# Performance work log

Measured on AMD Instinct MI355X. Metric: run time of the kernel, lower is better.

## Reference

```python
import jax, jax.numpy as jnp
import numpy as np

FACTOR = 3
N_HEADS = 8


def prob_attention(q, k, v, key):
    # q,k,v: [B, L, H, D]  (Informer ProbAttention, mask_flag falsy, scale=None)
    B, L_Q, H, D = q.shape
    L_K = k.shape[1]
    Q = jnp.swapaxes(q, 1, 2)  # [B,H,L_Q,D]
    K = jnp.swapaxes(k, 1, 2)
    V = jnp.swapaxes(v, 1, 2)
    U_part = min(FACTOR * int(np.ceil(np.log(L_K))), L_K)  # sampled keys per query
    u = min(FACTOR * int(np.ceil(np.log(L_Q))), L_Q)       # active (top) queries
    idx = jax.random.randint(key, (L_Q, U_part), 0, L_K)   # shared across B,H like torch.randint
    K_sample = K[:, :, idx, :]                              # [B,H,L_Q,U_part,D] gather
    QK_sample = jnp.einsum('bhld,bhlsd->bhls', Q, K_sample)
    M = QK_sample.max(axis=-1) - QK_sample.sum(axis=-1) / L_K  # sparsity measure
    _, top_idx = jax.lax.top_k(M, u)                        # [B,H,u]
    Q_reduce = jnp.take_along_axis(Q, top_idx[..., None], axis=2)  # [B,H,u,D]
    scale = 1.0 / np.sqrt(D)
    scores = jnp.einsum('bhud,bhkd->bhuk', Q_reduce, K) * scale     # [B,H,u,L_K]
    attn = jax.nn.softmax(scores, axis=-1)
    out_top = jnp.einsum('bhuk,bhkd->bhud', attn, V)
    # initial context: mean of V over keys, broadcast to every query position
    context = jnp.broadcast_to(V.mean(axis=2, keepdims=True), (B, H, L_Q, D))
    bi = jnp.arange(B)[:, None, None]
    hi = jnp.arange(H)[None, :, None]
    context = context.at[bi, hi, top_idx].set(out_top)
    return jnp.swapaxes(context, 1, 2)  # [B,L_Q,H,D]


def attention_layer(xq, xk, xv, wq, bq, wk, bk, wv, bv, wo, bo, key):
    B, Lq, dm = xq.shape
    Lk = xk.shape[1]
    dk = dm // N_HEADS
    q = (xq @ wq + bq).reshape(B, Lq, N_HEADS, dk)
    k = (xk @ wk + bk).reshape(B, Lk, N_HEADS, dk)
    v = (xv @ wv + bv).reshape(B, Lk, N_HEADS, dk)
    out = prob_attention(q, k, v, key).reshape(B, Lq, dm)
    return out @ wo + bo


def setup_inputs() -> dict:
    key = jax.random.key(0)
    ks = jax.random.split(key, 20)
    B, Ld, Lp, dm = 4, 4096, 4096, 512
    inp = {
        'xs': jax.random.normal(ks[0], (B, Ld + Lp, dm), jnp.float32),
        'xd': jax.random.normal(ks[1], (B, Ld, dm), jnp.float32),
        'xp': jax.random.normal(ks[2], (B, Lp, dm), jnp.float32),
    }
    names = ['w0q', 'w0k', 'w0v', 'w0o', 'b0q', 'b0k', 'b0v', 'b0o',
             'w1q', 'w1k', 'w1v', 'w1o', 'b1q', 'b1k', 'b1v', 'b1o']
    for i, n in enumerate(names):
        if n.startswith('w'):
            inp[n] = jax.random.normal(ks[3 + i], (dm, dm), jnp.float32) * 0.02
        else:
            inp[n] = jnp.zeros((dm,), jnp.float32)
    return inp


def reference(xs, xd, xp,
              w0q, w0k, w0v, w0o, b0q, b0k, b0v, b0o,
              w1q, w1k, w1v, w1o, b1q, b1k, b1v, b1o):
    # dropout layers are identity in eval mode
    xp2 = attention_layer(xp, xd, xd, w0q, b0q, w0k, b0k, w0v, b0v, w0o, b0o,
                          jax.random.key(42))
    xd2 = attention_layer(xd, xp2, xp2, w1q, b1q, w1k, b1k, w1v, b1v, w1o, b1o,
                          jax.random.key(43))
    return xs + jnp.concatenate([xd2, xp2], axis=1)
```

## Files before the change

### kernel.cpp

```cpp
#include <hip/hip_runtime.h>
#include <math.h>

#define NB 4
#define SEQ 4096
#define DM 512
#define NH 8
#define HD 64
#define UU 27
#define NIDX (SEQ*UU)
#define NC 32
#define CS 128
#define PSTRIDE 66

typedef unsigned int u32;
typedef unsigned short u16;
typedef __attribute__((ext_vector_type(8))) short short8;
typedef __attribute__((ext_vector_type(4))) short short4v;
typedef __attribute__((ext_vector_type(4))) float f32x4;

__host__ __device__ inline u32 rotl32(u32 x, u32 r){ return (x<<r)|(x>>(32u-r)); }

__host__ __device__ inline void threefry2x32(u32 k0, u32 k1, u32 x0, u32 x1, u32* o0, u32* o1)
{
  u32 ks[3] = { k0, k1, k0 ^ k1 ^ 0x1BD11BDAu };
  x0 += ks[0]; x1 += ks[1];
  const u32 rotA[4] = {13u,15u,26u,6u};
  const u32 rotB[4] = {17u,29u,16u,24u};
  for (int i = 0; i < 5; i++) {
    const u32* rot = (i & 1) ? rotB : rotA;
    for (int j = 0; j < 4; j++) { x0 += x1; x1 = rotl32(x1, rot[j]); x1 ^= x0; }
    x0 += ks[(i+1)%3];
    x1 += ks[(i+2)%3] + (u32)(i+1);
  }
  *o0 = x0; *o1 = x1;
}

__global__ __launch_bounds__(256) void gen_idx_kernel(u32 k2a, u32 k2b, int* __restrict__ idx)
{
  int i = blockIdx.x * 256 + threadIdx.x;
  if (i >= NIDX) return;
  u32 o0, o1;
  threefry2x32(k2a, k2b, 0u, (u32)i, &o0, &o1);
  idx[i] = (int)((o0 ^ o1) & (SEQ - 1));
}

__device__ inline u16 f2bf_rne(float f) {
  u32 u = __float_as_uint(f);
  return (u16)((u + 0x7fffu + ((u >> 16) & 1u)) >> 16);
}
__device__ inline void f2bf_split(float f, u16& hi, u16& lo) {
  u32 u = __float_as_uint(f);
  u16 h = (u16)(u >> 16);
  float hf = __uint_as_float(((u32)h) << 16);
  hi = h;
  lo = f2bf_rne(f - hf);
}

__global__ __launch_bounds__(256) void conv_split(const float* __restrict__ X,
                                                  u16* __restrict__ hi, u16* __restrict__ lo)
{
  long g = (long)blockIdx.x * 256 + threadIdx.x;
  float4 x0 = ((const float4*)X)[g * 2];
  float4 x1 = ((const float4*)X)[g * 2 + 1];
  union { short8 v; u16 s[8]; } h, l;
  float xv[8] = { x0.x, x0.y, x0.z, x0.w, x1.x, x1.y, x1.z, x1.w };
  #pragma unroll
  for (int e = 0; e < 8; e++) f2bf_split(xv[e], h.s[e], l.s[e]);
  ((short8*)hi)[g] = h.v;
  ((short8*)lo)[g]  = l.v;
}

struct WPtrs { const float* w[8]; };
__global__ __launch_bounds__(256) void convw_kernel(WPtrs wp, u16* __restrict__ outp)
{
  const int n  = blockIdx.x;
  const int wi = blockIdx.y;
  const float* W = wp.w[wi];
  u16* hi = outp + (long)wi * 262144 + n * DM;
  u16* lo = hi + 8L * 262144;
  for (int k = threadIdx.x; k < DM; k += 256) {
    u16 h, l;
    f2bf_split(W[(long)k * DM + n], h, l);
    hi[k] = h; lo[k] = l;
  }
}

__device__ inline void gld16(const u16* g, short* l) {
  __builtin_amdgcn_global_load_lds((const u32*)g, (u32*)l, 16, 0, 0);
}

__global__ __launch_bounds__(256) void gemm_bf(
    const u16* __restrict__ Ah, const u16* __restrict__ Al,
    const u16* __restrict__ Wh, const u16* __restrict__ Wl,
    const float* __restrict__ bias0, const float* __restrict__ bias1,
    float* __restrict__ C0, float* __restrict__ C1,
    const float* __restrict__ resid, int rowJump)
{
  __shared__ short LB[2][4][4096];

  const int t  = threadIdx.x;
  const int rb = blockIdx.x * 128;
  const int cb = blockIdx.y * 128;

  const int slot = (t & 7) ^ ((t >> 3) & 7);
  const int c8   = slot & 3;
  const int rloc = ((t >> 3) << 1) + (slot >> 2);
  const u16* sAh = Ah + (long)(rb + rloc) * DM + c8 * 8;
  const u16* sWh = Wh + (long)(cb + rloc) * DM + c8 * 8;
  const u16* sAl = Al + (long)(rb + rloc) * DM + c8 * 8;
  const u16* sWl = Wl + (long)(cb + rloc) * DM + c8 * 8;
  const int w512 = (t >> 6) * 512;

  const int lane = t & 63, wv = t >> 6;
  const int wm = (wv & 1) * 64, wn = (wv >> 1) * 64;
  const int fr = lane & 15, fq = lane >> 4;
  const int fsw = (fr >> 1) * 64 + ((((fr & 1) * 4 + fq) ^ (fr >> 1)) * 8);
  const int a_off = wm * 32 + fsw;
  const int b_off = wn * 32 + fsw;

  f32x4 acc[4][4];
  #pragma unroll
  for (int i = 0; i < 4; i++)
    #pragma unroll
    for (int j = 0; j < 4; j++) acc[i][j] = (f32x4)(0.f);

#define STAGE(buf, k0s) do { \
    gld16(sAh + (k0s),               &LB[buf][0][w512]); \
    gld16(sAh + (k0s) + 64 * DM,     &LB[buf][0][w512 + 2048]); \
    gld16(sWh + (k0s),               &LB[buf][1][w512]); \
    gld16(sWh + (k0s) + 64 * DM,     &LB[buf][1][w512 + 2048]); \
    gld16(sAl + (k0s),               &LB[buf][2][w512]); \
    gld16(sAl + (k0s) + 64 * DM,     &LB[buf][2][w512 + 2048]); \
    gld16(sWl + (k0s),               &LB[buf][3][w512]); \
    gld16(sWl + (k0s) + 64 * DM,     &LB[buf][3][w512 + 2048]); \
  } while (0)

  STAGE(0, 0);
  #pragma unroll 2
  for (int ks = 0; ks < 16; ks++) {
    const int cur = ks & 1;
    asm volatile("s_waitcnt vmcnt(0)" ::: "memory");
    __syncthreads();
    if (ks < 15) STAGE(cur ^ 1, (ks + 1) * 32);

    short8 a_hi[4], b_hi[4], a_lo[4], b_lo[4];
    #pragma unroll
    for (int i = 0; i < 4; i++) a_hi[i] = *(const short8*)&LB[cur][0][a_off + i * 512];
    #pragma unroll
    for (int j = 0; j < 4; j++) b_hi[j] = *(const short8*)&LB[cur][1][b_off + j * 512];
    #pragma unroll
    for (int i = 0; i < 4; i++) a_lo[i] = *(const short8*)&LB[cur][2][a_off + i * 512];
    #pragma unroll
    for (int j = 0; j < 4; j++) b_lo[j] = *(const short8*)&LB[cur][3][b_off + j * 512];

    #pragma unroll
    for (int i = 0; i < 4; i++)
      #pragma unroll
      for (int j = 0; j < 4; j++)
        acc[i][j] = __builtin_amdgcn_mfma_f32_16x16x32_bf16(a_hi[i], b_hi[j], acc[i][j], 0, 0, 0);
    #pragma unroll
    for (int i = 0; i < 4; i++)
      #pragma unroll
      for (int j = 0; j < 4; j++) {
        acc[i][j] = __builtin_amdgcn_mfma_f32_16x16x32_bf16(a_hi[i], b_lo[j], acc[i][j], 0, 0, 0);
        acc[i][j] = __builtin_amdgcn_mfma_f32_16x16x32_bf16(a_lo[i], b_hi[j], acc[i][j], 0, 0, 0);
      }
  }
#undef STAGE

  #pragma unroll
  for (int j = 0; j < 4; j++) {
    int col = cb + wn + j * 16 + fr;
    const float* bp = (col < DM) ? bias0 : bias1;
    float* Cp = (col < DM) ? C0 : C1;
    int cc = col & (DM - 1);
    float bv = bp[cc];
    #pragma unroll
    for (int i = 0; i < 4; i++) {
      int row0 = rb + wm + i * 16 + fq * 4;
      #pragma unroll
      for (int r = 0; r < 4; r++) {
        int row = row0 + r;
        long off = (long)row * DM + (long)(row >> 12) * rowJump + cc;
        float v = acc[i][j][r] + bv;
        if (resid) v += resid[off];
        Cp[off] = v;
      }
    }
  }
}

__global__ __launch_bounds__(256) void mscore_kernel(const float* __restrict__ Q, const float* __restrict__ K,
                                                     const int* __restrict__ idx, float* __restrict__ M)
{
  const int wl = threadIdx.x >> 6, lane = threadIdx.x & 63;
  const int bl = blockIdx.x * 4 + wl;
  const int b = bl >> 12, l = bl & (SEQ - 1);

  const float4* qp = (const float4*)(Q + (long)bl * DM + lane * 8);
  float4 q0 = qp[0], q1 = qp[1];

  const int* ip = idx + l * UU;
  int idxv = ip[lane < UU ? lane : 0];
  int chv = idxv >> 9;

  const float* kb = K + ((long)b << 12) * DM + lane * 8;
  float mx = -INFINITY, sm = 0.f;
  #pragma unroll 1
  for (int c = 0; c < 8; c++) {
    unsigned long long msk = __ballot(chv == c) & ((1ull << UU) - 1ull);
    while (msk) {
      int s = __builtin_ctzll(msk);
      msk &= msk - 1;
      int kl = __shfl(idxv, s, 64);
      const float4* kp = (const float4*)(kb + (long)kl * DM);
      float4 k0 = kp[0], k1 = kp[1];
      float dot;
      dot = q0.x * k0.x;
      dot = fmaf(q0.y, k0.y, dot); dot = fmaf(q0.z, k0.z, dot); dot = fmaf(q0.w, k0.w, dot);
      dot = fmaf(q1.x, k1.x, dot); dot = fmaf(q1.y, k1.y, dot);
      dot = fmaf(q1.z, k1.z, dot); dot = fmaf(q1.w, k1.w, dot);
      dot += __shfl_xor(dot, 1, 64);
      dot += __shfl_xor(dot, 2, 64);
      dot += __shfl_xor(dot, 4, 64);
      mx = fmaxf(mx, dot);
      sm += dot;
    }
  }
  if ((lane & 7) == 0) {
    int h = lane >> 3;
    M[(((long)b * NH + h) << 12) + l] = mx - sm * (1.0f / (float)SEQ);
  }
}

__global__ __launch_bounds__(256) void topk_kernel(const float* __restrict__ M, int* __restrict__ topidx)
{
  __shared__ float vals[SEQ];
  __shared__ float rv[256];
  __shared__ int   ri[256];
  const float* m = M + (long)blockIdx.x * SEQ;
  for (int i = threadIdx.x; i < SEQ; i += 256) vals[i] = m[i];
  __syncthreads();
  for (int it = 0; it < UU; it++) {
    float bv = -INFINITY; int bi = 0x7fffffff;
    for (int i = threadIdx.x; i < SEQ; i += 256) {
      float v = vals[i];
      if (v > bv) { bv = v; bi = i; }
    }
    rv[threadIdx.x] = bv; ri[threadIdx.x] = bi;
    __syncthreads();
    for (int s = 128; s > 0; s >>= 1) {
      if (threadIdx.x < s) {
        float ov = rv[threadIdx.x + s]; int oi = ri[threadIdx.x + s];
        if (ov > rv[threadIdx.x] || (ov == rv[threadIdx.x] && oi < ri[threadIdx.x])) {
          rv[threadIdx.x] = ov; ri[threadIdx.x] = oi;
        }
      }
      __syncthreads();
    }
    if (threadIdx.x == 0) { topidx[blockIdx.x * UU + it] = ri[0]; vals[ri[0]] = -INFINITY; }
    __syncthreads();
  }
}

__global__ __launch_bounds__(512) void vmean_partial(const float* __restrict__ V, float* __restrict__ vsum)
{
  int b = blockIdx.x >> 5, chunk = blockIdx.x & 31;
  int c = threadIdx.x;
  const float* p = V + ((long)b * SEQ + chunk * 128) * DM + c;
  float s = 0.f;
  for (int l = 0; l < 128; l++) s += p[(long)l * DM];
  atomicAdd(&vsum[b * DM + c], s);
}

__global__ __launch_bounds__(256) void attn_part(const float* __restrict__ Q, const float* __restrict__ K,
                                                 const float* __restrict__ V, const int* __restrict__ topidx,
                                                 float* __restrict__ partial)
{
  __shared__ float Qs[UU][HD];
  __shared__ float S[UU][CS];
  __shared__ float Vt[CS][HD];
  __shared__ float m_s[UU], l_s[UU];

  const int t = threadIdx.x;
  const int bh = blockIdx.x;
  const int chunk = blockIdx.y;
  const int b = bh >> 3, h = bh & 7;
  const long kbase = ((long)(b << 12) + chunk * CS) * DM + h * HD;
  const int* tp = topidx + bh * UU;

  for (int i = t; i < UU * HD; i += 256) {
    int u = i >> 6, d = i & 63;
    Qs[u][d] = Q[((long)(b << 12) + tp[u]) * DM + h * HD + d];
  }
  for (int i = t; i < CS * (HD / 4); i += 256) {
    int row = i >> 4, c4 = (i & 15) << 2;
    *(float4*)&Vt[row][c4] = *(const float4*)(V + kbase + (long)row * DM + c4);
  }
  __syncthreads();

  {
    const int l = t >> 1, half = t & 1, d0 = half * 32;
    const float* kp = K + kbase + (long)l * DM + d0;
    float4 kr[8];
    #pragma unroll
    for (int j = 0; j < 8; j++) kr[j] = *(const float4*)(kp + j * 4);
    #pragma unroll 1
    for (int u = 0; u < UU; u++) {
      const float4* qf = (const float4*)&Qs[u][d0];
      float dot = 0.f;
      #pragma unroll
      for (int j = 0; j < 8; j++) {
        float4 q = qf[j];
        dot = fmaf(q.x, kr[j].x, dot); dot = fmaf(q.y, kr[j].y, dot);
        dot = fmaf(q.z, kr[j].z, dot); dot = fmaf(q.w, kr[j].w, dot);
      }
      float tot = dot + __shfl_xor(dot, 1, 64);
      if (half == 0) S[u][l] = tot * 0.125f;
    }
  }
  __syncthreads();

  {
    const int u = t >> 3, il = t & 7;
    if (u < UU) {
      float mx = -INFINITY;
      for (int l = il; l < CS; l += 8) mx = fmaxf(mx, S[u][l]);
      #pragma unroll
      for (int m = 1; m < 8; m <<= 1) mx = fmaxf(mx, __shfl_xor(mx, m, 64));
      float ps = 0.f;
      for (int l = il; l < CS; l += 8) {
        float e = expf(S[u][l] - mx);
        S[u][l] = e;
        ps += e;
      }
      #pragma unroll
      for (int m = 1; m < 8; m <<= 1) ps += __shfl_xor(ps, m, 64);
      if (il == 0) { m_s[u] = mx; l_s[u] = ps; }
    }
  }
  __syncthreads();

  {
    const int d = t & 63, g = t >> 6;
    for (int u = g; u < UU; u += 4) {
      float acc = 0.f;
      #pragma unroll 4
      for (int l = 0; l < CS; l += 4) {
        float4 p4 = *(const float4*)&S[u][l];
        acc = fmaf(p4.x, Vt[l][d],     acc);
        acc = fmaf(p4.y, Vt[l + 1][d], acc);
        acc = fmaf(p4.z, Vt[l + 2][d], acc);
        acc = fmaf(p4.w, Vt[l + 3][d], acc);
      }
      float* pp = partial + (((long)bh * NC + chunk) * UU + u) * PSTRIDE;
      pp[2 + d] = acc;
      if (d == 0) { pp[0] = m_s[u]; pp[1] = l_s[u]; }
    }
  }
}

__global__ __launch_bounds__(64) void attn_merge_bf(const float* __restrict__ partial, const int* __restrict__ topidx,
                                                    u16* __restrict__ hi, u16* __restrict__ lo)
{
  int g = blockIdx.x;
  int bh = g / UU, u = g % UU;
  int b = bh >> 3, h = bh & 7;
  int d = threadIdx.x;
  float M = -INFINITY, S = 0.f, acc = 0.f;
  for (int c = 0; c < NC; c++) {
    const float* pp = partial + (((long)bh * NC + c) * UU + u) * PSTRIDE;
    float mc = pp[0], sc = pp[1], a = pp[2 + d];
    if (mc > M) {
      float r = expf(M - mc);
      acc *= r; S *= r; M = mc;
    }
    float w = expf(mc - M);
    acc = fmaf(a, w, acc);
    S = fmaf(sc, w, S);
  }
  int ql = topidx[g];
  long o = ((long)(b << 12) + ql) * DM + h * HD + d;
  u16 hv, lv;
  f2bf_split(acc / S, hv, lv);
  hi[o] = hv; lo[o] = lv;
}

__global__ __launch_bounds__(256) void ctx_fill_bf(const float* __restrict__ vsum,
                                                   u16* __restrict__ hi, u16* __restrict__ lo)
{
  long g = (long)blockIdx.x * 256 + threadIdx.x;
  int b = (int)(g >> 19);
  int c4 = (int)(g & 127);
  float4 v = ((const float4*)vsum)[b * 128 + c4];
  const float s = 1.0f / (float)SEQ;
  float xv[4] = { v.x * s, v.y * s, v.z * s, v.w * s };
  union { short4v v; u16 s[4]; } h, l;
  #pragma unroll
  for (int e = 0; e < 4; e++) f2bf_split(xv[e], h.s[e], l.s[e]);
  ((short4v*)hi)[g] = h.v;
  ((short4v*)lo)[g]  = l.v;
}

__global__ __launch_bounds__(256) void add_upper(const float* __restrict__ xs, const float* __restrict__ xp2,
                                                 float* __restrict__ out)
{
  long g = (long)blockIdx.x * 256 + threadIdx.x;
  int b = (int)(g >> 19);
  long rem = g & 524287;
  float4 p = ((const float4*)xp2)[g];
  long o = ((long)b * 8192 + SEQ) * 128 + rem;
  float4 x = ((const float4*)xs)[o];
  x.x += p.x; x.y += p.y; x.z += p.z; x.w += p.w;
  ((float4*)out)[o] = x;
}

extern "C" void kernel_launch(void* const* d_in, const int* in_sizes, int n_in,
                              void* d_out, int out_size, void* d_ws, size_t ws_size,
                              hipStream_t stream)
{
  const float* xs  = (const float*)d_in[0];
  const float* xd  = (const float*)d_in[1];
  const float* xp  = (const float*)d_in[2];
  const float* w0q = (const float*)d_in[3];
  const float* w0k = (const float*)d_in[4];
  const float* w0v = (const float*)d_in[5];
  const float* w0o = (const float*)d_in[6];
  const float* b0q = (const float*)d_in[7];
  const float* b0k = (const float*)d_in[8];
  const float* b0v = (const float*)d_in[9];
  const float* b0o = (const float*)d_in[10];
  const float* w1q = (const float*)d_in[11];
  const float* w1k = (const float*)d_in[12];
  const float* w1v = (const float*)d_in[13];
  const float* w1o = (const float*)d_in[14];
  const float* b1q = (const float*)d_in[15];
  const float* b1k = (const float*)d_in[16];
  const float* b1v = (const float*)d_in[17];
  const float* b1o = (const float*)d_in[18];
  float* out = (float*)d_out;

  const long BIG = (long)NB * SEQ * DM;
  float* A  = (float*)d_ws;
  float* Bb = A  + BIG;
  float* Cc = Bb + BIG;
  float* Dd = Cc + BIG;
  float* ex = Dd + BIG;
  float* Pq  = ex + BIG;
  float* Pkv = Pq + BIG;

  int*   idxbuf = (int*)ex;
  float* Mbuf   = ex + NIDX;
  int*   topidx = (int*)(Mbuf + (long)NB * NH * SEQ);
  float* vsum   = (float*)(topidx + NB * NH * UU);
  u16*   wpl    = (u16*)(ex + (1 << 20));

  u16* Pq_hi  = (u16*)Pq;   u16* Pq_lo  = Pq_hi  + BIG;
  u16* Pkv_hi = (u16*)Pkv;  u16* Pkv_lo = Pkv_hi + BIG;
  auto whi = [&](int i){ return wpl + (long)i * 262144; };
  auto wlo = [&](int i){ return wpl + 8L * 262144 + (long)i * 262144; };

  dim3 gg(128, 4);
  dim3 gkv(128, 8);
  dim3 ag(NB * NH, NC);
  u32 k2a, k2b;

  WPtrs wp;
  wp.w[0] = w0q; wp.w[1] = w0k; wp.w[2] = w0v; wp.w[3] = w0o;
  wp.w[4] = w1q; wp.w[5] = w1k; wp.w[6] = w1v; wp.w[7] = w1o;
  convw_kernel<<<dim3(512, 8), 256, 0, stream>>>(wp, wpl);

  threefry2x32(0u, 42u, 0u, 1u, &k2a, &k2b);
  gen_idx_kernel<<<(NIDX + 255) / 256, 256, 0, stream>>>(k2a, k2b, idxbuf);
  conv_split<<<4096, 256, 0, stream>>>(xp, Pq_hi, Pq_lo);
  conv_split<<<4096, 256, 0, stream>>>(xd, Pkv_hi, Pkv_lo);
  gemm_bf<<<gg, 256, 0, stream>>>(Pq_hi,  Pq_lo,  whi(0), wlo(0), b0q, b0q, A,  A,  nullptr, 0);
  gemm_bf<<<gkv, 256, 0, stream>>>(Pkv_hi, Pkv_lo, whi(1), wlo(1), b0k, b0v, Bb, Cc, nullptr, 0);
  mscore_kernel<<<NB * SEQ / 4, 256, 0, stream>>>(A, Bb, idxbuf, Mbuf);
  topk_kernel<<<NB * NH, 256, 0, stream>>>(Mbuf, topidx);
  hipMemsetAsync(vsum, 0, NB * DM * sizeof(float), stream);
  vmean_partial<<<NB * 32, 512, 0, stream>>>(Cc, vsum);
  attn_part<<<ag, 256, 0, stream>>>(A, Bb, Cc, topidx, Dd);
  ctx_fill_bf<<<8192, 256, 0, stream>>>(vsum, Pq_hi, Pq_lo);
  attn_merge_bf<<<NB * NH * UU, 64, 0, stream>>>(Dd, topidx, Pq_hi, Pq_lo);
  gemm_bf<<<gg, 256, 0, stream>>>(Pq_hi, Pq_lo, whi(3), wlo(3), b0o, b0o, Bb, Bb, nullptr, 0);
  add_upper<<<8192, 256, 0, stream>>>(xs, Bb, out);

  threefry2x32(0u, 43u, 0u, 1u, &k2a, &k2b);
  gen_idx_kernel<<<(NIDX + 255) / 256, 256, 0, stream>>>(k2a, k2b, idxbuf);
  gemm_bf<<<gg, 256, 0, stream>>>(Pkv_hi, Pkv_lo, whi(4), wlo(4), b1q, b1q, A, A, nullptr, 0);
  conv_split<<<4096, 256, 0, stream>>>(Bb, Pq_hi, Pq_lo);
  gemm_bf<<<gkv, 256, 0, stream>>>(Pq_hi, Pq_lo, whi(5), wlo(5), b1k, b1v, Cc, Dd, nullptr, 0);
  mscore_kernel<<<NB * SEQ / 4, 256, 0, stream>>>(A, Cc, idxbuf, Mbuf);
  topk_kernel<<<NB * NH, 256, 0, stream>>>(Mbuf, topidx);
  hipMemsetAsync(vsum, 0, NB * DM * sizeof(float), stream);
  vmean_partial<<<NB * 32, 512, 0, stream>>>(Dd, vsum);
  attn_part<<<ag, 256, 0, stream>>>(A, Cc, Dd, topidx, Bb);
  ctx_fill_bf<<<8192, 256, 0, stream>>>(vsum, Pkv_hi, Pkv_lo);
  attn_merge_bf<<<NB * NH * UU, 64, 0, stream>>>(Bb, topidx, Pkv_hi, Pkv_lo);
  gemm_bf<<<gg, 256, 0, stream>>>(Pkv_hi, Pkv_lo, whi(7), wlo(7), b1o, b1o, out, out, xs, SEQ * DM);
}
```

Measured before the change: 833.4 us.

## Deepen GEMM LDS pipeline to four stages and drop split precision where tolerable

Rewrites the bf16 split GEMM to keep four LDS stages in flight, using partial vmcnt waits and raw barriers, and raises wave priority around MFMA blocks. Adds a template switch that skips the low-part loads and cross-term MFMAs. That cheaper path is used for the second layer's V projection and its output projection, which splits the fused K/V GEMM in two. The high part now uses round-to-nearest, so the one-term product is more accurate. The aim is to hide load latency and cut MFMA work, at the cost of more LDS per block and lower precision on those GEMMs.

```diff
diff --git a/kernel.cpp b/kernel.cpp
--- a/kernel.cpp
+++ b/kernel.cpp
@@ -49,8 +49,7 @@
   return (u16)((u + 0x7fffu + ((u >> 16) & 1u)) >> 16);
 }
 __device__ inline void f2bf_split(float f, u16& hi, u16& lo) {
-  u32 u = __float_as_uint(f);
-  u16 h = (u16)(u >> 16);
+  u16 h = f2bf_rne(f);
   float hf = __uint_as_float(((u32)h) << 16);
   hi = h;
   lo = f2bf_rne(f - hf);
@@ -89,6 +88,7 @@
   __builtin_amdgcn_global_load_lds((const u32*)g, (u32*)l, 16, 0, 0);
 }
 
+template<int SPLIT>
 __global__ __launch_bounds__(256) void gemm_bf(
     const u16* __restrict__ Ah, const u16* __restrict__ Al,
     const u16* __restrict__ Wh, const u16* __restrict__ Wl,
@@ -96,7 +96,8 @@
     float* __restrict__ C0, float* __restrict__ C1,
     const float* __restrict__ resid, int rowJump)
 {
-  __shared__ short LB[2][4][4096];
+  __shared__ short LBh[4 * 8192];
+  __shared__ short LBl[SPLIT ? 4 * 8192 : 8];
 
   const int t  = threadIdx.x;
   const int rb = blockIdx.x * 128;
@@ -107,8 +108,8 @@
   const int rloc = ((t >> 3) << 1) + (slot >> 2);
   const u16* sAh = Ah + (long)(rb + rloc) * DM + c8 * 8;
   const u16* sWh = Wh + (long)(cb + rloc) * DM + c8 * 8;
-  const u16* sAl = Al + (long)(rb + rloc) * DM + c8 * 8;
-  const u16* sWl = Wl + (long)(cb + rloc) * DM + c8 * 8;
+  const u16* sAl = SPLIT ? (Al + (long)(rb + rloc) * DM + c8 * 8) : sAh;
+  const u16* sWl = SPLIT ? (Wl + (long)(cb + rloc) * DM + c8 * 8) : sWh;
   const int w512 = (t >> 6) * 512;
 
   const int lane = t & 63, wv = t >> 6;
@@ -124,49 +125,73 @@
     #pragma unroll
     for (int j = 0; j < 4; j++) acc[i][j] = (f32x4)(0.f);
 
-#define STAGE(buf, k0s) do { \
-    gld16(sAh + (k0s),               &LB[buf][0][w512]); \
-    gld16(sAh + (k0s) + 64 * DM,     &LB[buf][0][w512 + 2048]); \
-    gld16(sWh + (k0s),               &LB[buf][1][w512]); \
-    gld16(sWh + (k0s) + 64 * DM,     &LB[buf][1][w512 + 2048]); \
-    gld16(sAl + (k0s),               &LB[buf][2][w512]); \
-    gld16(sAl + (k0s) + 64 * DM,     &LB[buf][2][w512 + 2048]); \
-    gld16(sWl + (k0s),               &LB[buf][3][w512]); \
-    gld16(sWl + (k0s) + 64 * DM,     &LB[buf][3][w512 + 2048]); \
-  } while (0)
-
-  STAGE(0, 0);
-  #pragma unroll 2
-  for (int ks = 0; ks < 16; ks++) {
-    const int cur = ks & 1;
-    asm volatile("s_waitcnt vmcnt(0)" ::: "memory");
-    __syncthreads();
-    if (ks < 15) STAGE(cur ^ 1, (ks + 1) * 32);
-
-    short8 a_hi[4], b_hi[4], a_lo[4], b_lo[4];
+  auto stage = [&](int s, int k0s) {
+    short* dh = &LBh[s * 8192 + w512];
+    gld16(sAh + k0s,           dh);
+    gld16(sAh + k0s + 64 * DM, dh + 2048);
+    gld16(sWh + k0s,           dh + 4096);
+    gld16(sWh + k0s + 64 * DM, dh + 4096 + 2048);
+    if (SPLIT) {
+      short* dl = &LBl[s * 8192 + w512];
+      gld16(sAl + k0s,           dl);
+      gld16(sAl + k0s + 64 * DM, dl + 2048);
+      gld16(sWl + k0s,           dl + 4096);
+      gld16(sWl + k0s + 64 * DM, dl + 4096 + 2048);
+    }
+  };
+
+  auto compute = [&](int s) {
+    const short* bh = &LBh[s * 8192];
+    short8 a_hi[4], b_hi[4];
     #pragma unroll
-    for (int i = 0; i < 4; i++) a_hi[i] = *(const short8*)&LB[cur][0][a_off + i * 512];
+    for (int i = 0; i < 4; i++) a_hi[i] = *(const short8*)&bh[a_off + i * 512];
     #pragma unroll
-    for (int j = 0; j < 4; j++) b_hi[j] = *(const short8*)&LB[cur][1][b_off + j * 512];
-    #pragma unroll
-    for (int i = 0; i < 4; i++) a_lo[i] = *(const short8*)&LB[cur][2][a_off + i * 512];
-    #pragma unroll
-    for (int j = 0; j < 4; j++) b_lo[j] = *(const short8*)&LB[cur][3][b_off + j * 512];
-
+    for (int j = 0; j < 4; j++) b_hi[j] = *(const short8*)&bh[4096 + b_off + j * 512];
+    __builtin_amdgcn_s_setprio(1);
     #pragma unroll
     for (int i = 0; i < 4; i++)
       #pragma unroll
       for (int j = 0; j < 4; j++)
         acc[i][j] = __builtin_amdgcn_mfma_f32_16x16x32_bf16(a_hi[i], b_hi[j], acc[i][j], 0, 0, 0);
-    #pragma unroll
-    for (int i = 0; i < 4; i++)
-      #pragma unroll
-      for (int j = 0; j < 4; j++) {
-        acc[i][j] = __builtin_amdgcn_mfma_f32_16x16x32_bf16(a_hi[i], b_lo[j], acc[i][j], 0, 0, 0);
-        acc[i][j] = __builtin_amdgcn_mfma_f32_16x16x32_bf16(a_lo[i], b_hi[j], acc[i][j], 0, 0, 0);
-      }
-  }
-#undef STAGE
+    __builtin_amdgcn_s_setprio(0);
+    if (SPLIT) {
+      const short* bl = &LBl[s * 8192];
+      short8 a_lo[4], b_lo[4];
+      #pragma unroll
+      for (int i = 0; i < 4; i++) a_lo[i] = *(const short8*)&bl[a_off + i * 512];
+      #pragma unroll
+      for (int j = 0; j < 4; j++) b_lo[j] = *(const short8*)&bl[4096 + b_off + j * 512];
+      __builtin_amdgcn_s_setprio(1);
+      #pragma unroll
+      for (int i = 0; i < 4; i++)
+        #pragma unroll
+        for (int j = 0; j < 4; j++) {
+          acc[i][j] = __builtin_amdgcn_mfma_f32_16x16x32_bf16(a_hi[i], b_lo[j], acc[i][j], 0, 0, 0);
+          acc[i][j] = __builtin_amdgcn_mfma_f32_16x16x32_bf16(a_lo[i], b_hi[j], acc[i][j], 0, 0, 0);
+        }
+      __builtin_amdgcn_s_setprio(0);
+    }
+  };
+
+  stage(0, 0); stage(1, 32); stage(2, 64);
+
+  #pragma unroll
+  for (int k = 0; k < 14; ++k) {
+    if (SPLIT) asm volatile("s_waitcnt vmcnt(16)" ::: "memory");
+    else       asm volatile("s_waitcnt vmcnt(8)"  ::: "memory");
+    __builtin_amdgcn_s_barrier();
+    if (k < 13) stage((k + 3) & 3, (k + 3) * 32);
+    compute(k & 3);
+    asm volatile("s_waitcnt lgkmcnt(0)" ::: "memory");
+  }
+  if (SPLIT) asm volatile("s_waitcnt vmcnt(8)" ::: "memory");
+  else       asm volatile("s_waitcnt vmcnt(4)" ::: "memory");
+  __builtin_amdgcn_s_barrier();
+  compute(2);
+  asm volatile("s_waitcnt lgkmcnt(0)" ::: "memory");
+  asm volatile("s_waitcnt vmcnt(0)" ::: "memory");
+  __builtin_amdgcn_s_barrier();
+  compute(3);
 
   #pragma unroll
   for (int j = 0; j < 4; j++) {
@@ -474,8 +499,8 @@
   gen_idx_kernel<<<(NIDX + 255) / 256, 256, 0, stream>>>(k2a, k2b, idxbuf);
   conv_split<<<4096, 256, 0, stream>>>(xp, Pq_hi, Pq_lo);
   conv_split<<<4096, 256, 0, stream>>>(xd, Pkv_hi, Pkv_lo);
-  gemm_bf<<<gg, 256, 0, stream>>>(Pq_hi,  Pq_lo,  whi(0), wlo(0), b0q, b0q, A,  A,  nullptr, 0);
-  gemm_bf<<<gkv, 256, 0, stream>>>(Pkv_hi, Pkv_lo, whi(1), wlo(1), b0k, b0v, Bb, Cc, nullptr, 0);
+  gemm_bf<1><<<gg, 256, 0, stream>>>(Pq_hi,  Pq_lo,  whi(0), wlo(0), b0q, b0q, A,  A,  nullptr, 0);
+  gemm_bf<1><<<gkv, 256, 0, stream>>>(Pkv_hi, Pkv_lo, whi(1), wlo(1), b0k, b0v, Bb, Cc, nullptr, 0);
   mscore_kernel<<<NB * SEQ / 4, 256, 0, stream>>>(A, Bb, idxbuf, Mbuf);
   topk_kernel<<<NB * NH, 256, 0, stream>>>(Mbuf, topidx);
   hipMemsetAsync(vsum, 0, NB * DM * sizeof(float), stream);
@@ -483,14 +508,15 @@
   attn_part<<<ag, 256, 0, stream>>>(A, Bb, Cc, topidx, Dd);
   ctx_fill_bf<<<8192, 256, 0, stream>>>(vsum, Pq_hi, Pq_lo);
   attn_merge_bf<<<NB * NH * UU, 64, 0, stream>>>(Dd, topidx, Pq_hi, Pq_lo);
-  gemm_bf<<<gg, 256, 0, stream>>>(Pq_hi, Pq_lo, whi(3), wlo(3), b0o, b0o, Bb, Bb, nullptr, 0);
+  gemm_bf<1><<<gg, 256, 0, stream>>>(Pq_hi, Pq_lo, whi(3), wlo(3), b0o, b0o, Bb, Bb, nullptr, 0);
   add_upper<<<8192, 256, 0, stream>>>(xs, Bb, out);
 
   threefry2x32(0u, 43u, 0u, 1u, &k2a, &k2b);
   gen_idx_kernel<<<(NIDX + 255) / 256, 256, 0, stream>>>(k2a, k2b, idxbuf);
-  gemm_bf<<<gg, 256, 0, stream>>>(Pkv_hi, Pkv_lo, whi(4), wlo(4), b1q, b1q, A, A, nullptr, 0);
+  gemm_bf<1><<<gg, 256, 0, stream>>>(Pkv_hi, Pkv_lo, whi(4), wlo(4), b1q, b1q, A, A, nullptr, 0);
   conv_split<<<4096, 256, 0, stream>>>(Bb, Pq_hi, Pq_lo);
-  gemm_bf<<<gkv, 256, 0, stream>>>(Pq_hi, Pq_lo, whi(5), wlo(5), b1k, b1v, Cc, Dd, nullptr, 0);
+  gemm_bf<1><<<gg, 256, 0, stream>>>(Pq_hi, Pq_lo, whi(5), wlo(5), b1k, b1k, Cc, Cc, nullptr, 0);
+  gemm_bf<0><<<gg, 256, 0, stream>>>(Pq_hi, Pq_lo, whi(6), wlo(6), b1v, b1v, Dd, Dd, nullptr, 0);
   mscore_kernel<<<NB * SEQ / 4, 256, 0, stream>>>(A, Cc, idxbuf, Mbuf);
   topk_kernel<<<NB * NH, 256, 0, stream>>>(Mbuf, topidx);
   hipMemsetAsync(vsum, 0, NB * DM * sizeof(float), stream);
@@ -498,5 +524,5 @@
   attn_part<<<ag, 256, 0, stream>>>(A, Cc, Dd, topidx, Bb);
   ctx_fill_bf<<<8192, 256, 0, stream>>>(vsum, Pkv_hi, Pkv_lo);
   attn_merge_bf<<<NB * NH * UU, 64, 0, stream>>>(Bb, topidx, Pkv_hi, Pkv_lo);
-  gemm_bf<<<gg, 256, 0, stream>>>(Pkv_hi, Pkv_lo, whi(7), wlo(7), b1o, b1o, out, out, xs, SEQ * DM);
-}
+  gemm_bf<0><<<gg, 256, 0, stream>>>(Pkv_hi, Pkv_lo, whi(7), wlo(7), b1o, b1o, out, out, xs, SEQ * DM);
+}
```

Measured after the change: 882.9 us. 5.9% more time.

## Exploit low-rank context structure to replace output and K/V projection GEMMs

Applied to the files above, without the earlier changes.

The ProbAttention context is a per-batch constant row (the mean of V) except at the 27 selected query rows per head. The output projection therefore becomes one row-vector matmul per batch, plus sparse per-row corrections computed by small projection kernels, broadcast fills and atomic scatter-adds. The second layer's K/V projections reuse the same structure, applied to the first layer's output, so three full 16k×512×512 GEMMs and a conversion pass are replaced by small matvecs and scatters. The changes are that f2bf_split now rounds the high half to nearest, fp32 scalar matvecs replace the split-bf16 MFMA path for those terms, and scatter_add relies on float atomicAdd.

```diff
diff --git a/kernel.cpp b/kernel.cpp
--- a/kernel.cpp
+++ b/kernel.cpp
@@ -7,15 +7,16 @@
 #define NH 8
 #define HD 64
 #define UU 27
+#define NG (NB*NH*UU)
 #define NIDX (SEQ*UU)
 #define NC 32
 #define CS 128
 #define PSTRIDE 66
+#define GPB 8
 
 typedef unsigned int u32;
 typedef unsigned short u16;
 typedef __attribute__((ext_vector_type(8))) short short8;
-typedef __attribute__((ext_vector_type(4))) short short4v;
 typedef __attribute__((ext_vector_type(4))) float f32x4;
 
 __host__ __device__ inline u32 rotl32(u32 x, u32 r){ return (x<<r)|(x>>(32u-r)); }
@@ -49,8 +50,7 @@
   return (u16)((u + 0x7fffu + ((u >> 16) & 1u)) >> 16);
 }
 __device__ inline void f2bf_split(float f, u16& hi, u16& lo) {
-  u32 u = __float_as_uint(f);
-  u16 h = (u16)(u >> 16);
+  u16 h = f2bf_rne(f);
   float hf = __uint_as_float(((u32)h) << 16);
   hi = h;
   lo = f2bf_rne(f - hf);
@@ -70,7 +70,7 @@
   ((short8*)lo)[g]  = l.v;
 }
 
-struct WPtrs { const float* w[8]; };
+struct WPtrs { const float* w[4]; };
 __global__ __launch_bounds__(256) void convw_kernel(WPtrs wp, u16* __restrict__ outp)
 {
   const int n  = blockIdx.x;
@@ -93,8 +93,7 @@
     const u16* __restrict__ Ah, const u16* __restrict__ Al,
     const u16* __restrict__ Wh, const u16* __restrict__ Wl,
     const float* __restrict__ bias0, const float* __restrict__ bias1,
-    float* __restrict__ C0, float* __restrict__ C1,
-    const float* __restrict__ resid, int rowJump)
+    float* __restrict__ C0, float* __restrict__ C1)
 {
   __shared__ short LB[2][4][4096];
 
@@ -181,10 +180,7 @@
       #pragma unroll
       for (int r = 0; r < 4; r++) {
         int row = row0 + r;
-        long off = (long)row * DM + (long)(row >> 12) * rowJump + cc;
-        float v = acc[i][j][r] + bv;
-        if (resid) v += resid[off];
-        Cp[off] = v;
+        Cp[(long)row * DM + cc] = acc[i][j][r] + bv;
       }
     }
   }
@@ -360,12 +356,10 @@
   }
 }
 
-__global__ __launch_bounds__(64) void attn_merge_bf(const float* __restrict__ partial, const int* __restrict__ topidx,
-                                                    u16* __restrict__ hi, u16* __restrict__ lo)
+__global__ __launch_bounds__(64) void attn_merge_c(const float* __restrict__ partial, float* __restrict__ otop)
 {
   int g = blockIdx.x;
   int bh = g / UU, u = g % UU;
-  int b = bh >> 3, h = bh & 7;
   int d = threadIdx.x;
   float M = -INFINITY, S = 0.f, acc = 0.f;
   for (int c = 0; c < NC; c++) {
@@ -379,27 +373,102 @@
     acc = fmaf(a, w, acc);
     S = fmaf(sc, w, S);
   }
-  int ql = topidx[g];
-  long o = ((long)(b << 12) + ql) * DM + h * HD + d;
-  u16 hv, lv;
-  f2bf_split(acc / S, hv, lv);
-  hi[o] = hv; lo[o] = lv;
-}
-
-__global__ __launch_bounds__(256) void ctx_fill_bf(const float* __restrict__ vsum,
-                                                   u16* __restrict__ hi, u16* __restrict__ lo)
+  otop[(long)g * HD + d] = acc / S;
+}
+
+__global__ __launch_bounds__(256) void rowmv_kernel(const float* __restrict__ xin, float scale,
+                                                    const float* __restrict__ W, const float* __restrict__ bias,
+                                                    float* __restrict__ xout, float* __restrict__ ctx_store)
+{
+  int b = blockIdx.x;
+  __shared__ float x[DM];
+  for (int k = threadIdx.x; k < DM; k += 256) {
+    float v = xin[b * DM + k] * scale;
+    x[k] = v;
+    if (ctx_store) ctx_store[b * DM + k] = v;
+  }
+  __syncthreads();
+  for (int n0 = 0; n0 < DM; n0 += 256) {
+    int n = n0 + threadIdx.x;
+    float acc = bias[n];
+    for (int k = 0; k < DM; k++) acc = fmaf(x[k], W[(long)k * DM + n], acc);
+    xout[b * DM + n] = acc;
+  }
+}
+
+__global__ __launch_bounds__(256) void cproj_kernel(const float* __restrict__ otop, const float* __restrict__ base_ctx,
+                                                    const float* __restrict__ W, float* __restrict__ c)
+{
+  int g = blockIdx.x; int bh = g / UU; int b = bh >> 3, h = bh & 7;
+  __shared__ float dlt[HD];
+  if (threadIdx.x < HD)
+    dlt[threadIdx.x] = otop[(long)g * HD + threadIdx.x] - base_ctx[b * DM + h * HD + threadIdx.x];
+  __syncthreads();
+  for (int n0 = 0; n0 < DM; n0 += 256) {
+    int n = n0 + threadIdx.x;
+    float acc = 0.f;
+    #pragma unroll 8
+    for (int d = 0; d < HD; d++) acc = fmaf(dlt[d], W[(long)(h * HD + d) * DM + n], acc);
+    c[(long)g * DM + n] = acc;
+  }
+}
+
+__global__ __launch_bounds__(256) void fill_rows(const float* __restrict__ base, float* __restrict__ dst)
 {
   long g = (long)blockIdx.x * 256 + threadIdx.x;
   int b = (int)(g >> 19);
-  int c4 = (int)(g & 127);
-  float4 v = ((const float4*)vsum)[b * 128 + c4];
-  const float s = 1.0f / (float)SEQ;
-  float xv[4] = { v.x * s, v.y * s, v.z * s, v.w * s };
-  union { short4v v; u16 s[4]; } h, l;
-  #pragma unroll
-  for (int e = 0; e < 4; e++) f2bf_split(xv[e], h.s[e], l.s[e]);
-  ((short4v*)hi)[g] = h.v;
-  ((short4v*)lo)[g]  = l.v;
+  ((float4*)dst)[g] = ((const float4*)base)[b * 128 + (int)(g & 127)];
+}
+
+__global__ __launch_bounds__(256) void fill_rows_resid(const float* __restrict__ base, const float* __restrict__ xs,
+                                                       float* __restrict__ out)
+{
+  long g = (long)blockIdx.x * 256 + threadIdx.x;
+  int b = (int)(g >> 19);
+  long rem = g & 524287;
+  long o = (long)b * (8192 * 128) + rem;
+  float4 x = ((const float4*)xs)[o];
+  float4 v = ((const float4*)base)[b * 128 + (int)(g & 127)];
+  x.x += v.x; x.y += v.y; x.z += v.z; x.w += v.w;
+  ((float4*)out)[o] = x;
+}
+
+__global__ __launch_bounds__(256) void scatter_add(const float* __restrict__ c, const int* __restrict__ topidx,
+                                                   float* __restrict__ dst, int rowPitch)
+{
+  int g = blockIdx.x; int bh = g / UU, b = bh >> 3;
+  int ql = topidx[g];
+  float* row = dst + ((long)b * rowPitch + ql) * DM;
+  const float* cg = c + (long)g * DM;
+  for (int n = threadIdx.x; n < DM; n += 256) atomicAdd(&row[n], cg[n]);
+}
+
+__global__ __launch_bounds__(256) void proj_scatter(const float* __restrict__ c, const int* __restrict__ topidx,
+                                                    const float* __restrict__ W, float* __restrict__ dst)
+{
+  int g0 = blockIdx.x * GPB;
+  __shared__ float x[GPB][DM];
+  for (int i = threadIdx.x; i < GPB * DM; i += 256)
+    x[i >> 9][i & 511] = c[(long)g0 * DM + i];
+  __syncthreads();
+  for (int n0 = 0; n0 < DM; n0 += 256) {
+    int n = n0 + threadIdx.x;
+    float acc[GPB];
+    #pragma unroll
+    for (int j = 0; j < GPB; j++) acc[j] = 0.f;
+    for (int k = 0; k < DM; k++) {
+      float w = W[(long)k * DM + n];
+      #pragma unroll
+      for (int j = 0; j < GPB; j++) acc[j] = fmaf(x[j][k], w, acc[j]);
+    }
+    #pragma unroll
+    for (int j = 0; j < GPB; j++) {
+      int g = g0 + j;
+      int bh = g / UU, b = bh >> 3;
+      int ql = topidx[g];
+      atomicAdd(&dst[((long)b * SEQ + ql) * DM + n], acc[j]);
+    }
+  }
 }
 
 __global__ __launch_bounds__(256) void add_upper(const float* __restrict__ xs, const float* __restrict__ xp2,
@@ -449,11 +518,21 @@
   float* Pq  = ex + BIG;
   float* Pkv = Pq + BIG;
 
-  int*   idxbuf = (int*)ex;
-  float* Mbuf   = ex + NIDX;
-  int*   topidx = (int*)(Mbuf + (long)NB * NH * SEQ);
-  float* vsum   = (float*)(topidx + NB * NH * UU);
-  u16*   wpl    = (u16*)(ex + (1 << 20));
+  int*   idxbuf  = (int*)ex;
+  float* Mbuf    = ex + 131072;
+  int*   topidx0 = (int*)(ex + 262144);
+  int*   topidx1 = (int*)(ex + 263168);
+  float* vsum    = ex + 264192;
+  float* bctx0   = ex + 266240;
+  float* bout0   = ex + 268288;
+  float* bK1     = ex + 270336;
+  float* bV1     = ex + 272384;
+  float* bctx1   = ex + 274432;
+  float* bout1   = ex + 276480;
+  float* otop    = ex + 278528;
+  float* cbuf    = ex + (1L << 19);
+  u16*   wpl     = (u16*)(ex + (1L << 20));
+  float* partials= ex + 3L * (1L << 20);
 
   u16* Pq_hi  = (u16*)Pq;   u16* Pq_lo  = Pq_hi  + BIG;
   u16* Pkv_hi = (u16*)Pkv;  u16* Pkv_lo = Pkv_hi + BIG;
@@ -466,37 +545,44 @@
   u32 k2a, k2b;
 
   WPtrs wp;
-  wp.w[0] = w0q; wp.w[1] = w0k; wp.w[2] = w0v; wp.w[3] = w0o;
-  wp.w[4] = w1q; wp.w[5] = w1k; wp.w[6] = w1v; wp.w[7] = w1o;
-  convw_kernel<<<dim3(512, 8), 256, 0, stream>>>(wp, wpl);
+  wp.w[0] = w0q; wp.w[1] = w0k; wp.w[2] = w0v; wp.w[3] = w1q;
+  convw_kernel<<<dim3(512, 4), 256, 0, stream>>>(wp, wpl);
 
   threefry2x32(0u, 42u, 0u, 1u, &k2a, &k2b);
   gen_idx_kernel<<<(NIDX + 255) / 256, 256, 0, stream>>>(k2a, k2b, idxbuf);
   conv_split<<<4096, 256, 0, stream>>>(xp, Pq_hi, Pq_lo);
   conv_split<<<4096, 256, 0, stream>>>(xd, Pkv_hi, Pkv_lo);
-  gemm_bf<<<gg, 256, 0, stream>>>(Pq_hi,  Pq_lo,  whi(0), wlo(0), b0q, b0q, A,  A,  nullptr, 0);
-  gemm_bf<<<gkv, 256, 0, stream>>>(Pkv_hi, Pkv_lo, whi(1), wlo(1), b0k, b0v, Bb, Cc, nullptr, 0);
+  gemm_bf<<<gg,  256, 0, stream>>>(Pq_hi,  Pq_lo,  whi(0), wlo(0), b0q, b0q, A,  A);
+  gemm_bf<<<gkv, 256, 0, stream>>>(Pkv_hi, Pkv_lo, whi(1), wlo(1), b0k, b0v, Bb, Cc);
   mscore_kernel<<<NB * SEQ / 4, 256, 0, stream>>>(A, Bb, idxbuf, Mbuf);
-  topk_kernel<<<NB * NH, 256, 0, stream>>>(Mbuf, topidx);
+  topk_kernel<<<NB * NH, 256, 0, stream>>>(Mbuf, topidx0);
   hipMemsetAsync(vsum, 0, NB * DM * sizeof(float), stream);
   vmean_partial<<<NB * 32, 512, 0, stream>>>(Cc, vsum);
-  attn_part<<<ag, 256, 0, stream>>>(A, Bb, Cc, topidx, Dd);
-  ctx_fill_bf<<<8192, 256, 0, stream>>>(vsum, Pq_hi, Pq_lo);
-  attn_merge_bf<<<NB * NH * UU, 64, 0, stream>>>(Dd, topidx, Pq_hi, Pq_lo);
-  gemm_bf<<<gg, 256, 0, stream>>>(Pq_hi, Pq_lo, whi(3), wlo(3), b0o, b0o, Bb, Bb, nullptr, 0);
+  attn_part<<<ag, 256, 0, stream>>>(A, Bb, Cc, topidx0, partials);
+  attn_merge_c<<<NG, 64, 0, stream>>>(partials, otop);
+  rowmv_kernel<<<NB, 256, 0, stream>>>(vsum, 1.0f / (float)SEQ, w0o, b0o, bout0, bctx0);
+  cproj_kernel<<<NG, 256, 0, stream>>>(otop, bctx0, w0o, cbuf);
+  fill_rows<<<8192, 256, 0, stream>>>(bout0, Bb);
+  scatter_add<<<NG, 256, 0, stream>>>(cbuf, topidx0, Bb, SEQ);
   add_upper<<<8192, 256, 0, stream>>>(xs, Bb, out);
 
   threefry2x32(0u, 43u, 0u, 1u, &k2a, &k2b);
   gen_idx_kernel<<<(NIDX + 255) / 256, 256, 0, stream>>>(k2a, k2b, idxbuf);
-  gemm_bf<<<gg, 256, 0, stream>>>(Pkv_hi, Pkv_lo, whi(4), wlo(4), b1q, b1q, A, A, nullptr, 0);
-  conv_split<<<4096, 256, 0, stream>>>(Bb, Pq_hi, Pq_lo);
-  gemm_bf<<<gkv, 256, 0, stream>>>(Pq_hi, Pq_lo, whi(5), wlo(5), b1k, b1v, Cc, Dd, nullptr, 0);
+  gemm_bf<<<gg, 256, 0, stream>>>(Pkv_hi, Pkv_lo, whi(3), wlo(3), b1q, b1q, A, A);
+  rowmv_kernel<<<NB, 256, 0, stream>>>(bout0, 1.0f, w1k, b1k, bK1, nullptr);
+  rowmv_kernel<<<NB, 256, 0, stream>>>(bout0, 1.0f, w1v, b1v, bV1, nullptr);
+  fill_rows<<<8192, 256, 0, stream>>>(bK1, Cc);
+  fill_rows<<<8192, 256, 0, stream>>>(bV1, Dd);
+  proj_scatter<<<NG / GPB, 256, 0, stream>>>(cbuf, topidx0, w1k, Cc);
+  proj_scatter<<<NG / GPB, 256, 0, stream>>>(cbuf, topidx0, w1v, Dd);
   mscore_kernel<<<NB * SEQ / 4, 256, 0, stream>>>(A, Cc, idxbuf, Mbuf);
-  topk_kernel<<<NB * NH, 256, 0, stream>>>(Mbuf, topidx);
+  topk_kernel<<<NB * NH, 256, 0, stream>>>(Mbuf, topidx1);
   hipMemsetAsync(vsum, 0, NB * DM * sizeof(float), stream);
   vmean_partial<<<NB * 32, 512, 0, stream>>>(Dd, vsum);
-  attn_part<<<ag, 256, 0, stream>>>(A, Cc, Dd, topidx, Bb);
-  ctx_fill_bf<<<8192, 256, 0, stream>>>(vsum, Pkv_hi, Pkv_lo);
-  attn_merge_bf<<<NB * NH * UU, 64, 0, stream>>>(Bb, topidx, Pkv_hi, Pkv_lo);
-  gemm_bf<<<gg, 256, 0, stream>>>(Pkv_hi, Pkv_lo, whi(7), wlo(7), b1o, b1o, out, out, xs, SEQ * DM);
-}
+  attn_part<<<ag, 256, 0, stream>>>(A, Cc, Dd, topidx1, partials);
+  attn_merge_c<<<NG, 64, 0, stream>>>(partials, otop);
+  rowmv_kernel<<<NB, 256, 0, stream>>>(vsum, 1.0f / (float)SEQ, w1o, b1o, bout1, bctx1);
+  cproj_kernel<<<NG, 256, 0, stream>>>(otop, bctx1, w1o, cbuf);
+  fill_rows_resid<<<8192, 256, 0, stream>>>(bout1, xs, out);
+  scatter_add<<<NG, 256, 0, stream>>>(cbuf, topidx1, out, 8192);
+}
```

Result: slower. 1.147 ms (+37.6%).
